# Performance work log

Measured on AMD Instinct MI355X. Metric: run time of the kernel, lower is better.

## Reference

```python
import jax, jax.numpy as jnp
import numpy as np

B, S, D, H, SE, DE, DFF = 4, 1024, 1024, 16, 77, 768, 4096


def _ln(x, g, b, eps=1e-5):
    mu = jnp.mean(x, axis=-1, keepdims=True)
    var = jnp.mean((x - mu) ** 2, axis=-1, keepdims=True)
    return (x - mu) * jax.lax.rsqrt(var + eps) * g + b


def _split_heads(x, heads):
    b, s, d = x.shape
    return x.reshape(b, s, heads, d // heads).transpose(0, 2, 1, 3)  # b h s hd


def _attn(q, k, v, heads):
    # memory_efficient_attention equivalent: softmax(q k^T * scale) v, per head
    q, k, v = _split_heads(q, heads), _split_heads(k, heads), _split_heads(v, heads)
    scale = q.shape[-1] ** -0.5
    scores = jnp.einsum('bhqd,bhkd->bhqk', q, k) * scale
    probs = jax.nn.softmax(scores, axis=-1)
    o = jnp.einsum('bhqk,bhkd->bhqd', probs, v)
    b, h, s, hd = o.shape
    return o.transpose(0, 2, 1, 3).reshape(b, s, h * hd)


def _geglu_ff(x, w1, b1, w2, b2):
    proj = x @ w1 + b1
    a, gate = jnp.split(proj, 2, axis=-1)
    return (a * jax.nn.gelu(gate)) @ w2 + b2


def _forward(h1, h2, enc, wq, wk, wv, wqc, wo, bo, ln1g, ln1b, ln2g, ln2b,
             w2q, w2k, w2v, w2o, b2o, wff1, bff1, wff2, bff2):
    # norm1
    n1 = _ln(h1, ln1g[0], ln1b[0])
    n2 = _ln(h2, ln1g[1], ln1b[1])
    # dual-stream uni-direction attention (self + cross with swapped K/V)
    q1, k1, v1, q1c = n1 @ wq[0], n1 @ wk[0], n1 @ wv[0], n1 @ wqc[0]
    q2, k2, v2, q2c = n2 @ wq[1], n2 @ wk[1], n2 @ wv[1], n2 @ wqc[1]
    a1 = _attn(q1, k1, v1, H) + _attn(q1c, k2, v2, H)
    a2 = _attn(q2, k2, v2, H) + _attn(q2c, k1, v1, H)
    a1 = a1 @ wo[0] + bo[0]
    a2 = a2 @ wo[1] + bo[1]
    h1 = h1 + a1
    h2 = h2 + a2
    # cross attention to encoder states (attn2)
    n1 = _ln(h1, ln2g[0], ln2b[0])
    n2 = _ln(h2, ln2g[1], ln2b[1])
    c1 = _attn(n1 @ w2q[0], enc @ w2k[0], enc @ w2v[0], H) @ w2o[0] + b2o[0]
    c2 = _attn(n2 @ w2q[1], enc @ w2k[1], enc @ w2v[1], H) @ w2o[1] + b2o[1]
    h1 = h1 + c1
    h2 = h2 + c2
    # feed-forward (GEGLU), applied to norm2 output exactly as in source
    h1 = h1 + _geglu_ff(n1, wff1[0], bff1[0], wff2[0], bff2[0])
    h2 = h2 + _geglu_ff(n2, wff1[1], bff1[1], wff2[1], bff2[1])
    return (h1, h2)


def setup_inputs() -> dict:
    key = jax.random.key(0)
    ks = jax.random.split(key, 16)
    f = lambda k, shp: jax.random.normal(k, shp, jnp.float32) * 0.02
    return {
        'h1': jax.random.normal(ks[0], (B, S, D), jnp.float32),
        'h2': jax.random.normal(ks[1], (B, S, D), jnp.float32),
        'enc': jax.random.normal(ks[2], (B, SE, DE), jnp.float32),
        'wq': f(ks[3], (2, D, D)), 'wk': f(ks[4], (2, D, D)),
        'wv': f(ks[5], (2, D, D)), 'wqc': f(ks[6], (2, D, D)),
        'wo': f(ks[7], (2, D, D)), 'bo': jnp.zeros((2, D), jnp.float32),
        'ln1g': jnp.ones((2, D), jnp.float32), 'ln1b': jnp.zeros((2, D), jnp.float32),
        'ln2g': jnp.ones((2, D), jnp.float32), 'ln2b': jnp.zeros((2, D), jnp.float32),
        'w2q': f(ks[8], (2, D, D)), 'w2k': f(ks[9], (2, DE, D)),
        'w2v': f(ks[10], (2, DE, D)), 'w2o': f(ks[11], (2, D, D)),
        'b2o': jnp.zeros((2, D), jnp.float32),
        'wff1': f(ks[12], (2, D, 2 * DFF)), 'bff1': jnp.zeros((2, 2 * DFF), jnp.float32),
        'wff2': f(ks[13], (2, DFF, D)), 'bff2': jnp.zeros((2, D), jnp.float32),
    }


def reference(h1, h2, enc, wq, wk, wv, wqc, wo, bo, ln1g, ln1b, ln2g, ln2b,
              w2q, w2k, w2v, w2o, b2o, wff1, bff1, wff2, bff2):
    return _forward(h1, h2, enc, wq, wk, wv, wqc, wo, bo, ln1g, ln1b, ln2g, ln2b,
                    w2q, w2k, w2v, w2o, b2o, wff1, bff1, wff2, bff2)
```

## Files before the change

### kernel.cpp

```cpp
#include <hip/hip_runtime.h>

typedef unsigned short u16;
typedef short v8s __attribute__((ext_vector_type(8)));
typedef float v4f __attribute__((ext_vector_type(4)));

__device__ __forceinline__ float bf2f(u16 u) {
  union { unsigned u; float f; } c; c.u = ((unsigned)u) << 16; return c.f;
}
__device__ __forceinline__ u16 f2bf(float x) {
  union { float f; unsigned u; } c; c.f = x;
  unsigned r = c.u + 0x7fffu + ((c.u >> 16) & 1u);
  return (u16)(r >> 16);
}
__device__ __forceinline__ v4f vzero() { v4f z; z[0]=0.f; z[1]=0.f; z[2]=0.f; z[3]=0.f; return z; }
__device__ __forceinline__ v4f mfma16(v8s a, v8s b, v4f c) {
  return __builtin_amdgcn_mfma_f32_16x16x32_bf16(a, b, c, 0, 0, 0);
}
__device__ __forceinline__ void async_lds16(const void* g, void* l) {
  __builtin_amdgcn_global_load_lds((__attribute__((address_space(1))) void*)g,
                                   (__attribute__((address_space(3))) void*)l, 16, 0, 0);
}
__device__ __forceinline__ unsigned cvtpk(float lo, float hi) {
  unsigned r;
  asm("v_cvt_pk_bf16_f32 %0, %1, %2" : "=v"(r) : "v"(lo), "v"(hi));
  return r;
}
__device__ __forceinline__ float gelu_f(float x) {
  return 0.5f * x * (1.f + tanhf(0.7978845608028654f * (x + 0.044715f * x * x * x)));
}

__global__ void detect_k(const unsigned* __restrict__ p, unsigned* __restrict__ flag) {
  if (threadIdx.x == 0) {
    flag[0] = (p[0] == 0x3F803F80u) ? 1u : 0u;
    flag[1] = 0u;
  }
}

__global__ __launch_bounds__(256) void cvt_k(const unsigned* __restrict__ flag,
    const void* __restrict__ src, u16* __restrict__ dst, int n) {
  int i = (blockIdx.x * 256 + threadIdx.x) * 8;
  if (i >= n) return;
  if (*flag) {
    *(uint4*)(dst + i) = *(const uint4*)((const u16*)src + i);
  } else {
    const float* s = (const float*)src + i;
    #pragma unroll
    for (int j = 0; j < 8; ++j) dst[i + j] = f2bf(s[j]);
  }
}

__global__ __launch_bounds__(256) void tr_k(const unsigned* __restrict__ flag,
    const void* __restrict__ in, u16* __restrict__ out, int R, int C, long outZS) {
  __shared__ u16 tile[32][33];
  size_t zin = (size_t)blockIdx.z * R * C;
  size_t zout = (size_t)blockIdx.z * outZS;
  int c0 = blockIdx.x * 32, r0 = blockIdx.y * 32;
  int tx = threadIdx.x & 31, ty = threadIdx.x >> 5;
  unsigned isbf = *flag;
  const u16* inb = (const u16*)in + zin;
  const float* inf = (const float*)in + zin;
  #pragma unroll
  for (int i = ty; i < 32; i += 8) {
    size_t idx = (size_t)(r0 + i) * C + c0 + tx;
    tile[i][tx] = isbf ? inb[idx] : f2bf(inf[idx]);
  }
  __syncthreads();
  out += zout;
  #pragma unroll
  for (int i = ty; i < 32; i += 8) out[(size_t)(c0 + i) * R + r0 + tx] = tile[tx][i];
}

__global__ __launch_bounds__(256) void vtr_k(const u16* __restrict__ in, u16* __restrict__ out) {
  __shared__ u16 tile[32][33];
  int z = blockIdx.z >> 2, b = blockIdx.z & 3;
  const u16* ip = in + (size_t)z * 16777216 + (size_t)b * 4194304 + 2048;
  u16* op = out + (size_t)z * 4194304 + (size_t)b * 1048576;
  int k0 = blockIdx.x * 32, d0 = blockIdx.y * 32;
  int tx = threadIdx.x & 31, ty = threadIdx.x >> 5;
  #pragma unroll
  for (int i = ty; i < 32; i += 8)
    tile[i][tx] = ip[(size_t)(k0 + i) * 4096 + d0 + tx];
  __syncthreads();
  int sl = (((tx >> 3) & 1) << 4) | (((tx >> 2) & 1) << 3) | (((tx >> 4) & 1) << 2) | (tx & 3);
  #pragma unroll
  for (int i = ty; i < 32; i += 8)
    op[(size_t)(d0 + i) * 1024 + k0 + sl] = tile[tx][i];
}

__global__ __launch_bounds__(256) void ln_k(const unsigned* __restrict__ flag,
    const void* __restrict__ src0, const void* __restrict__ src1,
    const u16* __restrict__ gw, const u16* __restrict__ bw, u16* __restrict__ out) {
  int z = blockIdx.y;
  const void* src = z ? src1 : src0;
  out += (size_t)z * 4194304; gw += z * 1024; bw += z * 1024;
  int row = blockIdx.x, t = threadIdx.x;
  unsigned isbf = *flag;
  float4 v;
  if (isbf) {
    uint2 d = ((const uint2*)((const u16*)src + (size_t)row * 1024))[t];
    v.x = bf2f((u16)(d.x & 0xffffu)); v.y = bf2f((u16)(d.x >> 16));
    v.z = bf2f((u16)(d.y & 0xffffu)); v.w = bf2f((u16)(d.y >> 16));
  } else {
    v = ((const float4*)((const float*)src + (size_t)row * 1024))[t];
  }
  float s = v.x + v.y + v.z + v.w;
  float s2 = v.x * v.x + v.y * v.y + v.z * v.z + v.w * v.w;
  #pragma unroll
  for (int o = 32; o; o >>= 1) { s += __shfl_down(s, o); s2 += __shfl_down(s2, o); }
  __shared__ float red[8];
  int w = t >> 6;
  if ((t & 63) == 0) { red[w] = s; red[4 + w] = s2; }
  __syncthreads();
  if (t == 0) {
    red[0] = red[0] + red[1] + red[2] + red[3];
    red[4] = red[4] + red[5] + red[6] + red[7];
  }
  __syncthreads();
  float mu = red[0] * (1.f / 1024.f);
  float var = red[4] * (1.f / 1024.f) - mu * mu;
  float rstd = rsqrtf(var + 1e-5f);
  int c = t * 4;
  float xs[4] = { v.x, v.y, v.z, v.w };
  #pragma unroll
  for (int j = 0; j < 4; ++j) {
    float g = bf2f(gw[c + j]), bb = bf2f(bw[c + j]);
    out[(size_t)row * 1024 + c + j] = f2bf((xs[j] - mu) * rstd * g + bb);
  }
}

template<int EPI>
__global__ __launch_bounds__(256, 2) void gemm_bt(
    const u16* __restrict__ A, const u16* __restrict__ Bt,
    int M, int N, int K, int lda, int ldb, int ldc,
    const u16* __restrict__ bias, const u16* aux,
    float* __restrict__ resF, void* __restrict__ outB,
    long zsA, long zsB, long zsC, int zsBias,
    const void* rin0, const void* rin1,
    const unsigned* __restrict__ flagp)
{
  int z = blockIdx.z;
  A += (size_t)z * zsA;
  Bt += (size_t)z * zsB;
  size_t zc = (size_t)z * zsC;
  unsigned isbf = 0;
  if (EPI == 4 || EPI == 5) isbf = *flagp;
  const void* rin = (EPI == 5) ? (z ? rin1 : rin0) : nullptr;
  __shared__ alignas(16) u16 As[128 * 64];
  __shared__ alignas(16) u16 Bs[128 * 64];
  int tid = threadIdx.x;
  int lane = tid & 63, wave = tid >> 6;
  int l15 = lane & 15, l4 = lane >> 4;
  int wm = wave & 1, wn = wave >> 1;
  int lin = blockIdx.x + blockIdx.y * gridDim.x;
  int nxy = gridDim.x * gridDim.y;
  int sw = (lin & 7) * (nxy >> 3) + (lin >> 3);
  int bx = sw % gridDim.x, by = sw / gridDim.x;
  int m0 = bx * 128, n0 = by * 128;
  v4f acc[4][4];
  #pragma unroll
  for (int i = 0; i < 4; ++i)
    #pragma unroll
    for (int j = 0; j < 4; ++j) acc[i][j] = vzero();

  for (int k0 = 0; k0 < K; k0 += 64) {
    #pragma unroll
    for (int it = 0; it < 4; ++it) {
      int sidx = it * 256 + tid;
      int r = sidx >> 3, cs = (sidx & 7) * 8;
      int ra = m0 + r; if (ra > M - 1) ra = M - 1;
      async_lds16(A + (size_t)ra * lda + k0 + cs, As + (size_t)(it * 256 + wave * 64) * 8);
      async_lds16(Bt + (size_t)(n0 + r) * ldb + k0 + cs, Bs + (size_t)(it * 256 + wave * 64) * 8);
    }
    __syncthreads();
    #pragma unroll
    for (int ks = 0; ks < 2; ++ks) {
      v8s af[4], bfr[4];
      #pragma unroll
      for (int i = 0; i < 4; ++i) {
        af[i]  = *(const v8s*)(As + (wm * 64 + i * 16 + l15) * 64 + ks * 32 + l4 * 8);
        bfr[i] = *(const v8s*)(Bs + (wn * 64 + i * 16 + l15) * 64 + ks * 32 + l4 * 8);
      }
      #pragma unroll
      for (int i = 0; i < 4; ++i)
        #pragma unroll
        for (int j = 0; j < 4; ++j)
          acc[i][j] = mfma16(af[i], bfr[j], acc[i][j]);
    }
    __syncthreads();
  }
  #pragma unroll
  for (int mt = 0; mt < 4; ++mt) {
    #pragma unroll
    for (int r = 0; r < 4; ++r) {
      int gr = m0 + wm * 64 + mt * 16 + l4 * 4 + r;
      if (gr >= M) continue;
      size_t ri = (size_t)gr * ldc;
      size_t ro = zc + ri;
      #pragma unroll
      for (int nt = 0; nt < 4; ++nt) {
        int gc = n0 + wn * 64 + nt * 16 + l15;
        float v = acc[mt][nt][r];
        if (bias) v += bf2f(bias[(size_t)z * zsBias + gc]);
        if (EPI == 0) ((u16*)outB)[ro + gc] = f2bf(v);
        else if (EPI == 1) ((u16*)outB)[ro + gc] = f2bf(gelu_f(v));
        else if (EPI == 2) ((u16*)outB)[ro + gc] = f2bf(v * bf2f(aux[ro + gc]));
        else if (EPI == 3) resF[ro + gc] += v;
        else if (EPI == 5) {
          float h = isbf ? bf2f(((const u16*)rin)[ri + gc]) : ((const float*)rin)[ri + gc];
          resF[ro + gc] = h + v;
        } else {
          float o = resF[ro + gc] + v;
          if (isbf) ((u16*)outB)[ro + gc] = f2bf(o);
          else ((float*)outB)[ro + gc] = o;
        }
      }
    }
  }
}

template<int EPI>
__global__ __launch_bounds__(512, 2) void gemm256(
    const u16* __restrict__ A, const u16* __restrict__ Bt,
    int M, int N, int K, int lda, int ldb, int ldc,
    const u16* __restrict__ bias, const u16* aux, void* __restrict__ outB,
    long zsA, long zsB, long zsC, int zsBias)
{
  __shared__ alignas(16) u16 As[4][8192];
  __shared__ alignas(16) u16 Bs[4][8192];
  int z = blockIdx.z;
  A += (size_t)z * zsA;
  Bt += (size_t)z * zsB;
  size_t zc = (size_t)z * zsC;
  int tid = threadIdx.x, lane = tid & 63, wave = tid >> 6;
  int l15 = lane & 15, l4 = lane >> 4;
  int wm = wave >> 2, wn = wave & 3;
  int lin = blockIdx.x + blockIdx.y * gridDim.x;
  int nxy = gridDim.x * gridDim.y;
  int sw = (lin & 7) * (nxy >> 3) + (lin >> 3);
  int bx = sw % gridDim.x, by = sw / gridDim.x;
  int m0 = bx * 256, n0 = by * 256;
  int sa = l4 ^ ((l15 >> 1) & 3);
  int nG = K >> 5;

  v4f acc[8][4];
  #pragma unroll
  for (int i = 0; i < 8; ++i)
    #pragma unroll
    for (int j = 0; j < 4; ++j) acc[i][j] = vzero();

  auto stageA = [&](int g) {
    int sl = g & 3;
    #pragma unroll
    for (int l = 0; l < 2; ++l) {
      int sidx = l * 512 + tid;
      int r = sidx >> 2, c = sidx & 3;
      async_lds16(A + (size_t)(m0 + r) * lda + g * 32 + ((c ^ ((sidx >> 3) & 3)) * 8),
                  As[sl] + (size_t)(l * 512 + wave * 64) * 8);
    }
  };
  auto stageB = [&](int g) {
    int sl = g & 3;
    #pragma unroll
    for (int l = 0; l < 2; ++l) {
      int sidx = l * 512 + tid;
      int r = sidx >> 2, c = sidx & 3;
      async_lds16(Bt + (size_t)(n0 + r) * ldb + g * 32 + ((c ^ ((sidx >> 3) & 3)) * 8),
                  Bs[sl] + (size_t)(l * 512 + wave * 64) * 8);
    }
  };
  auto gate = [&](int cnt) {
    if (cnt >= 2)      asm volatile("s_waitcnt vmcnt(8)" ::: "memory");
    else if (cnt == 1) asm volatile("s_waitcnt vmcnt(4)" ::: "memory");
    else               asm volatile("s_waitcnt vmcnt(0)" ::: "memory");
    __builtin_amdgcn_sched_barrier(0);
  };

  stageA(0); stageB(0);
  if (1 < nG) { stageA(1); stageB(1); }
  if (2 < nG) { stageA(2); stageB(2); }
  gate((1 < nG) + (2 < nG));
  __builtin_amdgcn_s_barrier();

  auto kstep = [&](int t, int s0, int s1) {
    int g0 = 2 * t, g1 = 2 * t + 1;
    const u16* a0 = As[s0]; const u16* b0 = Bs[s0];
    const u16* a1 = As[s1]; const u16* b1 = Bs[s1];
    v8s af[4], bf[4];
    #pragma unroll
    for (int i = 0; i < 4; ++i) {
      af[i] = *(const v8s*)(a0 + ((wm * 128 + i * 16 + l15) * 4 + sa) * 8);
      bf[i] = *(const v8s*)(b0 + ((wn * 64 + i * 16 + l15) * 4 + sa) * 8);
    }
    if (g0 + 3 < nG) stageA(g0 + 3);
    __builtin_amdgcn_s_barrier();
    __builtin_amdgcn_s_setprio(1);
    #pragma unroll
    for (int i = 0; i < 4; ++i)
      #pragma unroll
      for (int j = 0; j < 4; ++j) acc[i][j] = mfma16(af[i], bf[j], acc[i][j]);
    __builtin_amdgcn_s_setprio(0);
    __builtin_amdgcn_s_barrier();
    #pragma unroll
    for (int i = 0; i < 4; ++i)
      af[i] = *(const v8s*)(a0 + ((wm * 128 + 64 + i * 16 + l15) * 4 + sa) * 8);
    if (g0 + 3 < nG) stageB(g0 + 3);
    __builtin_amdgcn_s_barrier();
    __builtin_amdgcn_s_setprio(1);
    #pragma unroll
    for (int i = 0; i < 4; ++i)
      #pragma unroll
      for (int j = 0; j < 4; ++j) acc[4 + i][j] = mfma16(af[i], bf[j], acc[4 + i][j]);
    __builtin_amdgcn_s_setprio(0);
    gate((g0 + 2 < nG) + (g0 + 3 < nG));
    __builtin_amdgcn_s_barrier();
    #pragma unroll
    for (int i = 0; i < 4; ++i) {
      af[i] = *(const v8s*)(a1 + ((wm * 128 + i * 16 + l15) * 4 + sa) * 8);
      bf[i] = *(const v8s*)(b1 + ((wn * 64 + i * 16 + l15) * 4 + sa) * 8);
    }
    if (g1 + 3 < nG) stageA(g1 + 3);
    __builtin_amdgcn_s_barrier();
    __builtin_amdgcn_s_setprio(1);
    #pragma unroll
    for (int i = 0; i < 4; ++i)
      #pragma unroll
      for (int j = 0; j < 4; ++j) acc[i][j] = mfma16(af[i], bf[j], acc[i][j]);
    __builtin_amdgcn_s_setprio(0);
    __builtin_amdgcn_s_barrier();
    #pragma unroll
    for (int i = 0; i < 4; ++i)
      af[i] = *(const v8s*)(a1 + ((wm * 128 + 64 + i * 16 + l15) * 4 + sa) * 8);
    if (g1 + 3 < nG) stageB(g1 + 3);
    __builtin_amdgcn_s_barrier();
    __builtin_amdgcn_s_setprio(1);
    #pragma unroll
    for (int i = 0; i < 4; ++i)
      #pragma unroll
      for (int j = 0; j < 4; ++j) acc[4 + i][j] = mfma16(af[i], bf[j], acc[4 + i][j]);
    __builtin_amdgcn_s_setprio(0);
    gate((g1 + 2 < nG) + (g1 + 3 < nG));
    __builtin_amdgcn_s_barrier();
  };

  int Ksteps = K >> 6;
  for (int t = 0; t < Ksteps; t += 2) {
    kstep(t, 0, 1);
    kstep(t + 1, 2, 3);
  }

  #pragma unroll
  for (int mi = 0; mi < 8; ++mi) {
    #pragma unroll
    for (int rr = 0; rr < 4; ++rr) {
      int gr = m0 + wm * 128 + mi * 16 + l4 * 4 + rr;
      size_t ro = zc + (size_t)gr * ldc;
      #pragma unroll
      for (int ni = 0; ni < 4; ++ni) {
        int gc = n0 + wn * 64 + ni * 16 + l15;
        float v = acc[mi][ni][rr];
        if (bias) v += bf2f(bias[(size_t)z * zsBias + gc]);
        if (EPI == 0) ((u16*)outB)[ro + gc] = f2bf(v);
        else if (EPI == 1) ((u16*)outB)[ro + gc] = f2bf(gelu_f(v));
        else ((u16*)outB)[ro + gc] = f2bf(v * bf2f(aux[ro + gc]));
      }
    }
  }
}

__global__ __launch_bounds__(256, 4) void flash_self_k(
    const u16* __restrict__ qkv, const u16* __restrict__ Vt, u16* __restrict__ O)
{
  __shared__ alignas(16) u16 Ksh[128 * 64];
  __shared__ alignas(16) u16 Vsh[64 * 128];
  int tid = threadIdx.x, lane = tid & 63, wave = tid >> 6;
  int l15 = lane & 15, l4 = (lane >> 4) & 3;
  int lin = blockIdx.x + (blockIdx.y << 4) + (blockIdx.z << 8);
  int sw = (lin & 7) * 256 + (lin >> 3);
  int qblk = sw & 15, h = (sw >> 4) & 15, zb = sw >> 8;
  int strm = zb >> 2, b = zb & 3;
  const size_t ZS = 16777216;
  const size_t BS = 4194304;
  int q0 = qblk * 64 + wave * 16;
  int swz = l15 & 7;
  v4f res[4];
  #pragma unroll
  for (int i = 0; i < 4; ++i) res[i] = vzero();

  for (int sg = 0; sg < 2; ++sg) {
    int qcol = sg ? 3072 : 0;
    int ksrc = sg ? (strm ^ 1) : strm;
    const u16* Qb = qkv + (size_t)strm * ZS + (size_t)b * BS + qcol + h * 64;
    const u16* Kb = qkv + (size_t)ksrc * ZS + (size_t)b * BS + 1024 + h * 64;
    const u16* Vb = Vt + (size_t)ksrc * BS + (size_t)b * 1048576 + h * 65536;
    v8s qf0 = *(const v8s*)(Qb + (size_t)(q0 + l15) * 4096 + l4 * 8);
    v8s qf1 = *(const v8s*)(Qb + (size_t)(q0 + l15) * 4096 + l4 * 8 + 32);
    v4f oacc[4];
    #pragma unroll
    for (int i = 0; i < 4; ++i) oacc[i] = vzero();
    float mrun = -1e30f, lrun = 0.f;

    for (int c0 = 0; c0 < 1024; c0 += 128) {
      #pragma unroll
      for (int it = 0; it < 4; ++it) {
        int sidx = it * 256 + tid;
        int r = sidx >> 3, c = sidx & 7;
        async_lds16(Kb + (size_t)(c0 + r) * 4096 + ((c ^ (r & 7)) * 8),
                    Ksh + (size_t)(it * 256 + wave * 64) * 8);
      }
      #pragma unroll
      for (int it = 0; it < 4; ++it) {
        int sidx = it * 256 + tid;
        int d = sidx >> 4, c = sidx & 15;
        async_lds16(Vb + (size_t)d * 1024 + c0 + ((c ^ (d & 15)) * 8),
                    Vsh + (size_t)(it * 256 + wave * 64) * 8);
      }
      __syncthreads();
      v4f s[4][2];
      #pragma unroll
      for (int g = 0; g < 4; ++g) { s[g][0] = vzero(); s[g][1] = vzero(); }
      __builtin_amdgcn_s_setprio(1);
      #pragma unroll
      for (int g = 0; g < 4; ++g) {
        int rb0 = (g * 32 + l15) * 64, rb1 = rb0 + 16 * 64;
        v8s k00 = *(const v8s*)(Ksh + rb0 + ((l4 ^ swz) * 8));
        v8s k10 = *(const v8s*)(Ksh + rb1 + ((l4 ^ swz) * 8));
        v8s k01 = *(const v8s*)(Ksh + rb0 + (((4 + l4) ^ swz) * 8));
        v8s k11 = *(const v8s*)(Ksh + rb1 + (((4 + l4) ^ swz) * 8));
        s[g][0] = mfma16(k00, qf0, s[g][0]);
        s[g][1] = mfma16(k10, qf0, s[g][1]);
        s[g][0] = mfma16(k01, qf1, s[g][0]);
        s[g][1] = mfma16(k11, qf1, s[g][1]);
      }
      __builtin_amdgcn_s_setprio(0);
      float tm = -1e30f;
      #pragma unroll
      for (int g = 0; g < 4; ++g)
        #pragma unroll
        for (int hh = 0; hh < 2; ++hh)
          #pragma unroll
          for (int r = 0; r < 4; ++r) {
            s[g][hh][r] *= 0.125f;
            tm = fmaxf(tm, s[g][hh][r]);
          }
      tm = fmaxf(tm, __shfl_xor(tm, 16));
      tm = fmaxf(tm, __shfl_xor(tm, 32));
      float alpha = 1.f;
      if (!__all(tm <= mrun + 8.f)) {
        float mn = fmaxf(mrun, tm);
        alpha = __expf(mrun - mn);
        mrun = mn;
        #pragma unroll
        for (int r = 0; r < 4; ++r) {
          float ar = __shfl(alpha, l4 * 4 + r);
          #pragma unroll
          for (int nt = 0; nt < 4; ++nt) oacc[nt][r] *= ar;
        }
      }
      float rs = 0.f;
      unsigned pk[4][4];
      #pragma unroll
      for (int g = 0; g < 4; ++g)
        #pragma unroll
        for (int hh = 0; hh < 2; ++hh) {
          float p0 = __expf(s[g][hh][0] - mrun);
          float p1 = __expf(s[g][hh][1] - mrun);
          float p2 = __expf(s[g][hh][2] - mrun);
          float p3 = __expf(s[g][hh][3] - mrun);
          rs += (p0 + p1) + (p2 + p3);
          pk[g][hh * 2]     = cvtpk(p0, p1);
          pk[g][hh * 2 + 1] = cvtpk(p2, p3);
        }
      rs += __shfl_xor(rs, 16);
      rs += __shfl_xor(rs, 32);
      lrun = lrun * alpha + rs;
      __builtin_amdgcn_s_setprio(1);
      #pragma unroll
      for (int g = 0; g < 4; ++g) {
        union { unsigned u[4]; v8s v; } pa;
        pa.u[0] = pk[g][0]; pa.u[1] = pk[g][1]; pa.u[2] = pk[g][2]; pa.u[3] = pk[g][3];
        #pragma unroll
        for (int nt = 0; nt < 4; ++nt) {
          int vr = nt * 16 + l15;
          v8s vb = *(const v8s*)(Vsh + vr * 128 + (((g * 4 + l4) ^ (vr & 15)) * 8));
          oacc[nt] = mfma16(pa.v, vb, oacc[nt]);
        }
      }
      __builtin_amdgcn_s_setprio(0);
      __syncthreads();
    }
    #pragma unroll
    for (int r = 0; r < 4; ++r) {
      float lr = __shfl(lrun, l4 * 4 + r);
      float inv = 1.f / lr;
      #pragma unroll
      for (int nt = 0; nt < 4; ++nt) res[nt][r] += oacc[nt][r] * inv;
    }
  }
  #pragma unroll
  for (int nt = 0; nt < 4; ++nt) {
    #pragma unroll
    for (int r = 0; r < 4; ++r) {
      int gq = q0 + l4 * 4 + r;
      size_t oi = (size_t)strm * BS + ((size_t)b * 1024 + gq) * 1024 + h * 64 + nt * 16 + l15;
      O[oi] = f2bf(res[nt][r]);
    }
  }
}

__global__ __launch_bounds__(256, 2) void flash_cross_k(
    const u16* __restrict__ Q, const u16* __restrict__ KV, u16* __restrict__ O)
{
  __shared__ alignas(16) u16 Ksh[128 * 64];
  __shared__ alignas(16) unsigned VshT[64 * 68];
  __shared__ alignas(16) u16 Psh[4][16 * 128];
  int tid = threadIdx.x, lane = tid & 63, wave = tid >> 6;
  int l15 = lane & 15, l4 = lane >> 4;
  int h = blockIdx.y;
  int strm = blockIdx.z >> 2, b = blockIdx.z & 3;
  const u16* Qb = Q + (size_t)strm * 4194304 + (size_t)b * 1048576 + h * 64;
  const u16* Kb = KV + (size_t)strm * 630784 + (size_t)b * 157696 + h * 64;
  const u16* Vb = Kb + 1024;
  int q0 = blockIdx.x * 64 + wave * 16;
  u16* pw = Psh[wave];
  int swz = l15 & 7;
  v8s qf0 = *(const v8s*)(Qb + (size_t)(q0 + l15) * 1024 + l4 * 8);
  v8s qf1 = *(const v8s*)(Qb + (size_t)(q0 + l15) * 1024 + l4 * 8 + 32);

  #pragma unroll
  for (int it = 0; it < 4; ++it) {
    int sidx = it * 256 + tid;
    int r = sidx >> 3, c = sidx & 7;
    int gk = r > 76 ? 76 : r;
    async_lds16(Kb + (size_t)gk * 2048 + ((c ^ (r & 7)) * 8),
                Ksh + (size_t)(it * 256 + wave * 64) * 8);
  }
  #pragma unroll
  for (int it = 0; it < 2; ++it) {
    int tt = it * 256 + tid;
    int kp = tt & 63, dsg = tt >> 6;
    int gk0 = kp * 2, gk1 = kp * 2 + 1;
    if (gk0 > 76) gk0 = 76;
    if (gk1 > 76) gk1 = 76;
    v8s v0 = *(const v8s*)(Vb + (size_t)gk0 * 2048 + dsg * 8);
    v8s v1 = *(const v8s*)(Vb + (size_t)gk1 * 2048 + dsg * 8);
    #pragma unroll
    for (int j = 0; j < 8; ++j) {
      unsigned pk = (unsigned)(u16)v0[j] | ((unsigned)(u16)v1[j] << 16);
      VshT[(dsg * 8 + j) * 68 + kp] = pk;
    }
  }
  __syncthreads();
  v4f s[4][2];
  #pragma unroll
  for (int g = 0; g < 4; ++g) { s[g][0] = vzero(); s[g][1] = vzero(); }
  __builtin_amdgcn_s_setprio(1);
  #pragma unroll
  for (int g = 0; g < 4; ++g) {
    int rb0 = (g * 32 + l15) * 64, rb1 = rb0 + 16 * 64;
    v8s k00 = *(const v8s*)(Ksh + rb0 + ((l4 ^ swz) * 8));
    v8s k10 = *(const v8s*)(Ksh + rb1 + ((l4 ^ swz) * 8));
    v8s k01 = *(const v8s*)(Ksh + rb0 + (((4 + l4) ^ swz) * 8));
    v8s k11 = *(const v8s*)(Ksh + rb1 + (((4 + l4) ^ swz) * 8));
    s[g][0] = mfma16(qf0, k00, s[g][0]);
    s[g][1] = mfma16(qf0, k10, s[g][1]);
    s[g][0] = mfma16(qf1, k01, s[g][0]);
    s[g][1] = mfma16(qf1, k11, s[g][1]);
  }
  __builtin_amdgcn_s_setprio(0);
  float lsum[4];
  #pragma unroll
  for (int r = 0; r < 4; ++r) {
    int row = l4 * 4 + r;
    float x[8];
    #pragma unroll
    for (int g = 0; g < 4; ++g) {
      bool ok0 = (g * 32 + l15) < 77, ok1 = (g * 32 + 16 + l15) < 77;
      x[2 * g]     = ok0 ? s[g][0][r] * 0.125f : -1e30f;
      x[2 * g + 1] = ok1 ? s[g][1][r] * 0.125f : -1e30f;
    }
    float tm = fmaxf(fmaxf(fmaxf(x[0], x[1]), fmaxf(x[2], x[3])),
                     fmaxf(fmaxf(x[4], x[5]), fmaxf(x[6], x[7])));
    #pragma unroll
    for (int o = 8; o; o >>= 1) tm = fmaxf(tm, __shfl_xor(tm, o));
    float rs = 0.f;
    #pragma unroll
    for (int j = 0; j < 8; ++j) {
      float p = __expf(x[j] - tm);
      rs += p;
      int col = (j >> 1) * 32 + (j & 1) * 16 + l15;
      pw[row * 128 + (((col >> 3) ^ row) * 8) + (col & 7)] = f2bf(p);
    }
    #pragma unroll
    for (int o = 8; o; o >>= 1) rs += __shfl_xor(rs, o);
    lsum[r] = rs;
  }
  v4f oacc[4];
  #pragma unroll
  for (int i = 0; i < 4; ++i) oacc[i] = vzero();
  __builtin_amdgcn_s_setprio(1);
  #pragma unroll
  for (int g = 0; g < 4; ++g) {
    v8s pa = *(const v8s*)(pw + l15 * 128 + (((g * 4 + l4) ^ l15) * 8));
    #pragma unroll
    for (int nt = 0; nt < 4; ++nt) {
      v8s vb = *(const v8s*)((const u16*)VshT + (nt * 16 + l15) * 136 + g * 32 + l4 * 8);
      oacc[nt] = mfma16(pa, vb, oacc[nt]);
    }
  }
  __builtin_amdgcn_s_setprio(0);
  #pragma unroll
  for (int nt = 0; nt < 4; ++nt) {
    #pragma unroll
    for (int r = 0; r < 4; ++r) {
      int gq = q0 + l4 * 4 + r;
      size_t oi = (size_t)strm * 4194304 + ((size_t)b * 1024 + gq) * 1024 + h * 64 + nt * 16 + l15;
      O[oi] = f2bf(oacc[nt][r] / lsum[r]);
    }
  }
}

extern "C" void kernel_launch(void* const* d_in, const int* in_sizes, int n_in,
                              void* d_out, int out_size, void* d_ws, size_t ws_size,
                              hipStream_t stream)
{
  (void)in_sizes; (void)n_in; (void)out_size;
  const void* h1   = d_in[0];
  const void* h2   = d_in[1];
  const void* enc  = d_in[2];
  const void* wq   = d_in[3];
  const void* wk   = d_in[4];
  const void* wv   = d_in[5];
  const void* wqc  = d_in[6];
  const void* wo   = d_in[7];
  const void* bo   = d_in[8];
  const void* ln1g = d_in[9];
  const void* ln1b = d_in[10];
  const void* ln2g = d_in[11];
  const void* ln2b = d_in[12];
  const void* w2q  = d_in[13];
  const void* w2k  = d_in[14];
  const void* w2v  = d_in[15];
  const void* w2o  = d_in[16];
  const void* b2o  = d_in[17];
  const void* wff1 = d_in[18];
  const void* bff1 = d_in[19];
  const void* wff2 = d_in[20];
  const void* bff2 = d_in[21];

  const size_t S1 = 4194304;
  const size_t W1 = 1048576;
  const size_t QS = 16777216;
  const size_t NE = 236544;

  char* base = (char*)d_ws;
  size_t off = 0;
  auto AL = [&](size_t n) { size_t r = off; off += (n + 255) & ~(size_t)255; return r; };
  size_t o_flag   = AL(256);
  size_t o_pb     = AL(30720 * 2);
  size_t o_encB   = AL(NE * 2);
  size_t o_wqkvT  = AL(2 * 4 * W1 * 2);
  size_t o_woT    = AL(2 * W1 * 2);
  size_t o_w2qT   = AL(2 * W1 * 2);
  size_t o_w2oT   = AL(2 * W1 * 2);
  size_t o_w2kvT  = AL(2 * 2048 * 768 * 2);
  size_t o_wff1T  = AL(2 * 8192 * 1024 * 2);
  size_t o_wff2T  = AL(2 * 4096 * 1024 * 2);
  size_t o_hw     = AL(2 * S1 * 4);
  size_t o_n      = AL(2 * S1 * 2);
  size_t o_qkv    = AL(2 * QS * 2);
  size_t o_ab     = AL(2 * S1 * 2);
  if (ws_size < off) return;

  unsigned* flagp = (unsigned*)(base + o_flag);
  const unsigned* zerop = flagp + 1;
  u16* pb = (u16*)(base + o_pb);
  u16* boB   = pb + 0;
  u16* b2oB  = pb + 2048;
  u16* ln1gB = pb + 4096;
  u16* ln1bB = pb + 6144;
  u16* ln2gB = pb + 8192;
  u16* ln2bB = pb + 10240;
  u16* bff2B = pb + 12288;
  u16* bff1B = pb + 14336;
  u16* encB  = (u16*)(base + o_encB);
  u16* wqkvT = (u16*)(base + o_wqkvT);
  u16* woT   = (u16*)(base + o_woT);
  u16* w2qT  = (u16*)(base + o_w2qT);
  u16* w2oT  = (u16*)(base + o_w2oT);
  u16* w2kvT = (u16*)(base + o_w2kvT);
  u16* wff1T = (u16*)(base + o_wff1T);
  u16* wff2T = (u16*)(base + o_wff2T);
  float* hw  = (float*)(base + o_hw);
  u16* n1    = (u16*)(base + o_n);
  u16* qkv   = (u16*)(base + o_qkv);
  u16* a1b   = (u16*)(base + o_ab);
  u16* q1x   = qkv;
  u16* c1b   = qkv + 2 * S1;
  u16* kencv = qkv + 4 * S1;
  u16* gelu  = qkv;
  u16* vtb   = n1;

  auto tr = [&](const void* ip, u16* op, int R, int C, long outZS) {
    dim3 g(C / 32, R / 32, 2);
    tr_k<<<g, 256, 0, stream>>>(flagp, ip, op, R, C, outZS);
  };
  auto cvt = [&](const void* ip, u16* op, int n) {
    cvt_k<<<(n / 8 + 255) / 256, 256, 0, stream>>>(flagp, ip, op, n);
  };
  auto gemm = [&](int epi, const u16* Ap, const u16* Bp, int M, int N, int K,
                  int lda, int ldb, int ldc, const u16* bias, const u16* aux,
                  float* resF, void* oB, int nz, long zsA, long zsB, long zsC, int zsBias,
                  const void* rin0, const void* rin1) {
    dim3 g((M + 127) / 128, N / 128, nz);
    switch (epi) {
      case 0: gemm_bt<0><<<g, 256, 0, stream>>>(Ap, Bp, M, N, K, lda, ldb, ldc, bias, aux, resF, oB, zsA, zsB, zsC, zsBias, rin0, rin1, flagp); break;
      case 1: gemm_bt<1><<<g, 256, 0, stream>>>(Ap, Bp, M, N, K, lda, ldb, ldc, bias, aux, resF, oB, zsA, zsB, zsC, zsBias, rin0, rin1, flagp); break;
      case 2: gemm_bt<2><<<g, 256, 0, stream>>>(Ap, Bp, M, N, K, lda, ldb, ldc, bias, aux, resF, oB, zsA, zsB, zsC, zsBias, rin0, rin1, flagp); break;
      case 3: gemm_bt<3><<<g, 256, 0, stream>>>(Ap, Bp, M, N, K, lda, ldb, ldc, bias, aux, resF, oB, zsA, zsB, zsC, zsBias, rin0, rin1, flagp); break;
      case 4: gemm_bt<4><<<g, 256, 0, stream>>>(Ap, Bp, M, N, K, lda, ldb, ldc, bias, aux, resF, oB, zsA, zsB, zsC, zsBias, rin0, rin1, flagp); break;
      default: gemm_bt<5><<<g, 256, 0, stream>>>(Ap, Bp, M, N, K, lda, ldb, ldc, bias, aux, resF, oB, zsA, zsB, zsC, zsBias, rin0, rin1, flagp); break;
    }
  };

  detect_k<<<1, 64, 0, stream>>>((const unsigned*)ln1g, flagp);
  cvt(bo, boB, 2048);     cvt(b2o, b2oB, 2048);
  cvt(ln1g, ln1gB, 2048); cvt(ln1b, ln1bB, 2048);
  cvt(ln2g, ln2gB, 2048); cvt(ln2b, ln2bB, 2048);
  cvt(bff2, bff2B, 2048); cvt(bff1, bff1B, 16384);
  cvt(enc, encB, (int)NE);
  tr(wq,  wqkvT + 0 * W1, 1024, 1024, 4 * (long)W1);
  tr(wk,  wqkvT + 1 * W1, 1024, 1024, 4 * (long)W1);
  tr(wv,  wqkvT + 2 * W1, 1024, 1024, 4 * (long)W1);
  tr(wqc, wqkvT + 3 * W1, 1024, 1024, 4 * (long)W1);
  tr(wo,  woT,  1024, 1024, (long)W1);
  tr(w2q, w2qT, 1024, 1024, (long)W1);
  tr(w2o, w2oT, 1024, 1024, (long)W1);
  tr(w2k, w2kvT + 0,          768, 1024, 2048L * 768);
  tr(w2v, w2kvT + 1024 * 768, 768, 1024, 2048L * 768);
  tr(wff1, wff1T, 1024, 8192, 8192L * 1024);
  tr(wff2, wff2T, 4096, 1024, 4096L * 1024);
  ln_k<<<dim3(4096, 2), 256, 0, stream>>>(flagp, h1, h2, ln1gB, ln1bB, n1);
  gemm256<0><<<dim3(16, 16, 2), 512, 0, stream>>>(n1, wqkvT, 4096, 4096, 1024,
      1024, 1024, 4096, nullptr, nullptr, qkv, (long)S1, 4 * (long)W1, (long)QS, 0);
  vtr_k<<<dim3(32, 32, 8), 256, 0, stream>>>(qkv, vtb);
  flash_self_k<<<dim3(16, 16, 8), 256, 0, stream>>>(qkv, vtb, a1b);
  gemm(5, a1b, woT, 4096, 1024, 1024, 1024, 1024, 1024, boB, nullptr, hw, nullptr,
       2, (long)S1, (long)W1, (long)S1, 1024, h1, h2);
  ln_k<<<dim3(4096, 2), 256, 0, stream>>>(zerop, hw, hw + S1, ln2gB, ln2bB, n1);
  gemm(0, n1, w2qT, 4096, 1024, 1024, 1024, 1024, 1024, nullptr, nullptr, nullptr, q1x,
       2, (long)S1, (long)W1, (long)S1, 0, nullptr, nullptr);
  gemm(0, encB, w2kvT, 308, 2048, 768, 768, 768, 2048, nullptr, nullptr, nullptr, kencv,
       2, 0, 2048L * 768, 308L * 2048, 0, nullptr, nullptr);
  flash_cross_k<<<dim3(16, 16, 8), 256, 0, stream>>>(q1x, kencv, c1b);
  gemm(3, c1b, w2oT, 4096, 1024, 1024, 1024, 1024, 1024, b2oB, nullptr, hw, nullptr,
       2, (long)S1, (long)W1, (long)S1, 1024, nullptr, nullptr);
  gemm256<1><<<dim3(16, 16, 2), 512, 0, stream>>>(n1, wff1T + 4096 * 1024, 4096, 4096, 1024,
      1024, 1024, 4096, bff1B + 4096, nullptr, gelu, (long)S1, 8192L * 1024, (long)QS, 8192);
  gemm256<2><<<dim3(16, 16, 2), 512, 0, stream>>>(n1, wff1T, 4096, 4096, 1024,
      1024, 1024, 4096, bff1B, gelu, gelu, (long)S1, 8192L * 1024, (long)QS, 8192);
  gemm(4, gelu, wff2T, 4096, 1024, 4096, 4096, 4096, 1024,
       bff2B, nullptr, hw, d_out, 2, (long)QS, 4096L * 1024, (long)S1, 1024,
       nullptr, nullptr);
}
```

Baseline: 1.133 ms.

## Restructure GEMM main loop with double-buffered register fragments and merged staging

```diff
diff --git a/kernel.cpp b/kernel.cpp
--- a/kernel.cpp
+++ b/kernel.cpp
@@ -248,23 +248,16 @@
     #pragma unroll
     for (int j = 0; j < 4; ++j) acc[i][j] = vzero();
 
-  auto stageA = [&](int g) {
+  auto stage = [&](int g) {
     int sl = g & 3;
     #pragma unroll
     for (int l = 0; l < 2; ++l) {
       int sidx = l * 512 + tid;
       int r = sidx >> 2, c = sidx & 3;
-      async_lds16(A + (size_t)(m0 + r) * lda + g * 32 + ((c ^ ((sidx >> 3) & 3)) * 8),
+      int cs = (c ^ ((sidx >> 3) & 3)) * 8;
+      async_lds16(A + (size_t)(m0 + r) * lda + g * 32 + cs,
                   As[sl] + (size_t)(l * 512 + wave * 64) * 8);
-    }
-  };
-  auto stageB = [&](int g) {
-    int sl = g & 3;
-    #pragma unroll
-    for (int l = 0; l < 2; ++l) {
-      int sidx = l * 512 + tid;
-      int r = sidx >> 2, c = sidx & 3;
-      async_lds16(Bt + (size_t)(n0 + r) * ldb + g * 32 + ((c ^ ((sidx >> 3) & 3)) * 8),
+      async_lds16(Bt + (size_t)(n0 + r) * ldb + g * 32 + cs,
                   Bs[sl] + (size_t)(l * 512 + wave * 64) * 8);
     }
   };
@@ -274,78 +267,59 @@
     else               asm volatile("s_waitcnt vmcnt(0)" ::: "memory");
     __builtin_amdgcn_sched_barrier(0);
   };
-
-  stageA(0); stageB(0);
-  if (1 < nG) { stageA(1); stageB(1); }
-  if (2 < nG) { stageA(2); stageB(2); }
+  v8s FA[8], FB[8], Bf[4];
+  auto dsA = [&](v8s* F, int u) {
+    const u16* a = As[u & 3];
+    #pragma unroll
+    for (int i = 0; i < 8; ++i)
+      F[i] = *(const v8s*)(a + ((wm * 128 + i * 16 + l15) * 4 + sa) * 8);
+  };
+  auto dsB = [&](int u) {
+    const u16* bp = Bs[u & 3];
+    #pragma unroll
+    for (int j = 0; j < 4; ++j)
+      Bf[j] = *(const v8s*)(bp + ((wn * 64 + j * 16 + l15) * 4 + sa) * 8);
+  };
+  auto lgk = [&](bool more) {
+    if (more) asm volatile("s_waitcnt lgkmcnt(8)" ::: "memory");
+    else      asm volatile("s_waitcnt lgkmcnt(0)" ::: "memory");
+    __builtin_amdgcn_sched_barrier(0);
+  };
+  auto mfma_blk = [&](v8s* F) {
+    __builtin_amdgcn_s_setprio(1);
+    #pragma unroll
+    for (int i = 0; i < 8; ++i)
+      #pragma unroll
+      for (int j = 0; j < 4; ++j) acc[i][j] = mfma16(F[i], Bf[j], acc[i][j]);
+    __builtin_amdgcn_s_setprio(0);
+  };
+
+  stage(0);
+  if (1 < nG) stage(1);
+  if (2 < nG) stage(2);
   gate((1 < nG) + (2 < nG));
   __builtin_amdgcn_s_barrier();
-
-  auto kstep = [&](int t, int s0, int s1) {
-    int g0 = 2 * t, g1 = 2 * t + 1;
-    const u16* a0 = As[s0]; const u16* b0 = Bs[s0];
-    const u16* a1 = As[s1]; const u16* b1 = Bs[s1];
-    v8s af[4], bf[4];
-    #pragma unroll
-    for (int i = 0; i < 4; ++i) {
-      af[i] = *(const v8s*)(a0 + ((wm * 128 + i * 16 + l15) * 4 + sa) * 8);
-      bf[i] = *(const v8s*)(b0 + ((wn * 64 + i * 16 + l15) * 4 + sa) * 8);
-    }
-    if (g0 + 3 < nG) stageA(g0 + 3);
+  dsA(FA, 0);
+
+  for (int u = 0; u < nG; u += 2) {
+    if (u + 3 < nG) stage(u + 3);
+    gate((u + 2 < nG) + (u + 3 < nG));
     __builtin_amdgcn_s_barrier();
-    __builtin_amdgcn_s_setprio(1);
-    #pragma unroll
-    for (int i = 0; i < 4; ++i)
-      #pragma unroll
-      for (int j = 0; j < 4; ++j) acc[i][j] = mfma16(af[i], bf[j], acc[i][j]);
-    __builtin_amdgcn_s_setprio(0);
+    dsB(u);
+    if (u + 1 < nG) dsA(FB, u + 1);
+    lgk(u + 1 < nG);
+    mfma_blk(FA);
     __builtin_amdgcn_s_barrier();
-    #pragma unroll
-    for (int i = 0; i < 4; ++i)
-      af[i] = *(const v8s*)(a0 + ((wm * 128 + 64 + i * 16 + l15) * 4 + sa) * 8);
-    if (g0 + 3 < nG) stageB(g0 + 3);
-    __builtin_amdgcn_s_barrier();
-    __builtin_amdgcn_s_setprio(1);
-    #pragma unroll
-    for (int i = 0; i < 4; ++i)
-      #pragma unroll
-      for (int j = 0; j < 4; ++j) acc[4 + i][j] = mfma16(af[i], bf[j], acc[4 + i][j]);
-    __builtin_amdgcn_s_setprio(0);
-    gate((g0 + 2 < nG) + (g0 + 3 < nG));
-    __builtin_amdgcn_s_barrier();
-    #pragma unroll
-    for (int i = 0; i < 4; ++i) {
-      af[i] = *(const v8s*)(a1 + ((wm * 128 + i * 16 + l15) * 4 + sa) * 8);
-      bf[i] = *(const v8s*)(b1 + ((wn * 64 + i * 16 + l15) * 4 + sa) * 8);
-    }
-    if (g1 + 3 < nG) stageA(g1 + 3);
-    __builtin_amdgcn_s_barrier();
-    __builtin_amdgcn_s_setprio(1);
-    #pragma unroll
-    for (int i = 0; i < 4; ++i)
-      #pragma unroll
-      for (int j = 0; j < 4; ++j) acc[i][j] = mfma16(af[i], bf[j], acc[i][j]);
-    __builtin_amdgcn_s_setprio(0);
-    __builtin_amdgcn_s_barrier();
-    #pragma unroll
-    for (int i = 0; i < 4; ++i)
-      af[i] = *(const v8s*)(a1 + ((wm * 128 + 64 + i * 16 + l15) * 4 + sa) * 8);
-    if (g1 + 3 < nG) stageB(g1 + 3);
-    __builtin_amdgcn_s_barrier();
-    __builtin_amdgcn_s_setprio(1);
-    #pragma unroll
-    for (int i = 0; i < 4; ++i)
-      #pragma unroll
-      for (int j = 0; j < 4; ++j) acc[4 + i][j] = mfma16(af[i], bf[j], acc[4 + i][j]);
-    __builtin_amdgcn_s_setprio(0);
-    gate((g1 + 2 < nG) + (g1 + 3 < nG));
-    __builtin_amdgcn_s_barrier();
-  };
-
-  int Ksteps = K >> 6;
-  for (int t = 0; t < Ksteps; t += 2) {
-    kstep(t, 0, 1);
-    kstep(t + 1, 2, 3);
+    if (u + 1 < nG) {
+      if (u + 4 < nG) stage(u + 4);
+      gate((u + 3 < nG) + (u + 4 < nG));
+      __builtin_amdgcn_s_barrier();
+      dsB(u + 1);
+      if (u + 2 < nG) dsA(FA, u + 2);
+      lgk(u + 2 < nG);
+      mfma_blk(FB);
+      __builtin_amdgcn_s_barrier();
+    }
   }
 
   #pragma unroll
```

After: 1.198 ms. 5.8% more time.
